# Kernel tuning notes

Measured on AMD Instinct MI355X. Metric: run time of the kernel, lower is better.

Reference implementation:

```python
import jax, jax.numpy as jnp
import numpy as np

D_MODEL = 1024
N_HEADS = 16
D_FF = 2 * D_MODEL
EPS = 1e-6


def setup_inputs() -> dict:
    key = jax.random.key(0)
    ks = jax.random.split(key, 12)
    B, S, D = 2, 2048, D_MODEL
    w = lambda k, shape: (jax.random.normal(k, shape, dtype=jnp.float32) * 0.02)
    return {
        "x": jax.random.normal(ks[0], (B, S, D), dtype=jnp.float32),
        "mask": jnp.ones((B, S, S), dtype=jnp.int32),
        "alpha1": jnp.ones((D,), jnp.float32),
        "bias1": jnp.zeros((D,), jnp.float32),
        "Wq": w(ks[1], (D, D)), "bq": jnp.zeros((D,), jnp.float32),
        "Wk": w(ks[2], (D, D)), "bk": jnp.zeros((D,), jnp.float32),
        "Wv": w(ks[3], (D, D)), "bv": jnp.zeros((D,), jnp.float32),
        "Wo": w(ks[4], (D, D)), "bo": jnp.zeros((D,), jnp.float32),
        "alpha2": jnp.ones((D,), jnp.float32),
        "bias2": jnp.zeros((D,), jnp.float32),
        "W1": w(ks[5], (D, D_FF)), "b1": jnp.zeros((D_FF,), jnp.float32),
        "W2": w(ks[6], (D_FF, D)), "b2": jnp.zeros((D,), jnp.float32),
    }


def _norm(x, alpha, bias):
    # torch: alpha*(x-mean)/(std+eps)+bias, std is unbiased (ddof=1)
    mu = jnp.mean(x, axis=-1, keepdims=True)
    sd = jnp.std(x, axis=-1, ddof=1, keepdims=True)
    return alpha * (x - mu) / (sd + EPS) + bias


def _gelu(x):
    return jax.nn.gelu(x, approximate=False)  # torch F.gelu exact


def _attention(x2, mask, Wq, bq, Wk, bk, Wv, bv, Wo, bo):
    B, S, D = x2.shape
    h, dk = N_HEADS, D // N_HEADS
    # project and split heads: [B, h, S, dk]
    q = (x2 @ Wq + bq).reshape(B, S, h, dk).transpose(0, 2, 1, 3)
    k = (x2 @ Wk + bk).reshape(B, S, h, dk).transpose(0, 2, 1, 3)
    v = (x2 @ Wv + bv).reshape(B, S, h, dk).transpose(0, 2, 1, 3)
    scores = jnp.einsum('bhqd,bhkd->bhqk', q, k) / np.sqrt(dk).astype(np.float32)
    scores = jnp.where(mask[:, None] == 0, jnp.float32(-1e9), scores)
    attn = jax.nn.softmax(scores, axis=-1)
    out = jnp.einsum('bhqk,bhkd->bhqd', attn, v)
    out = out.transpose(0, 2, 1, 3).reshape(B, S, D)
    return out @ Wo + bo


def reference(x, mask, alpha1, bias1, Wq, bq, Wk, bk, Wv, bv, Wo, bo,
              alpha2, bias2, W1, b1, W2, b2):
    x2 = _norm(x, alpha1, bias1)
    x = x + _attention(x2, mask, Wq, bq, Wk, bk, Wv, bv, Wo, bo)
    x2 = _norm(x, alpha2, bias2)
    ff = _gelu(_gelu(x2 @ W1 + b1) @ W2 + b2)
    return x + ff
```

## Files before the change

kernel.cpp:

```cpp
#include <hip/hip_runtime.h>
#include <math.h>

typedef __attribute__((ext_vector_type(8))) short v8s;
typedef __attribute__((ext_vector_type(4))) float v4f;
typedef __attribute__((ext_vector_type(2))) float v2f;
typedef __attribute__((ext_vector_type(16))) float v16f;
typedef __attribute__((ext_vector_type(4))) unsigned int v4u;
typedef __attribute__((ext_vector_type(2))) unsigned int v2u;

#define MFMA16(a,b,c) __builtin_amdgcn_mfma_f32_16x16x32_bf16(a,b,c,0,0,0)
#define MFMA32(a,b,c) __builtin_amdgcn_mfma_f32_32x32x16_bf16(a,b,c,0,0,0)
#define QSCALE 0.18033688011112042f

typedef const __attribute__((address_space(1))) void* gp1_t;
typedef __attribute__((address_space(3))) void* lp3_t;
__device__ __forceinline__ void gll16(const void* g, void* l){
  __builtin_amdgcn_global_load_lds((gp1_t)g, (lp3_t)l, 16, 0, 0);
}
#define VMCNT(n) asm volatile("s_waitcnt vmcnt(" #n ")" ::: "memory")

__device__ __forceinline__ unsigned short f2b(float f){
  unsigned u = __builtin_bit_cast(unsigned, f);
  u += 0x7FFFu + ((u>>16)&1u);
  return (unsigned short)(u>>16);
}
__device__ __forceinline__ float b2f(unsigned short u){
  return __builtin_bit_cast(float, ((unsigned)u)<<16);
}
__device__ __forceinline__ unsigned cvtpk(float lo, float hi){
  unsigned r;
  asm("v_cvt_pk_bf16_f32 %0, %1, %2" : "=v"(r) : "v"(lo), "v"(hi));
  return r;
}
__device__ __forceinline__ float gelu_exact(float x){
  return 0.5f*x*(1.0f + erff(x*0.70710678118654752f));
}

__global__ __launch_bounds__(256) void ln_kernel(const float* __restrict__ x,
    const float* __restrict__ alpha, const float* __restrict__ bias,
    unsigned short* __restrict__ out)
{
  const int D = 1024;
  int row = blockIdx.x;
  int tid = threadIdx.x;
  const float* xr = x + (size_t)row*D;
  v4f v = ((const v4f*)xr)[tid];
  float s  = v[0]+v[1]+v[2]+v[3];
  float s2 = v[0]*v[0]+v[1]*v[1]+v[2]*v[2]+v[3]*v[3];
  #pragma unroll
  for (int off=1; off<64; off<<=1){ s += __shfl_xor(s, off); s2 += __shfl_xor(s2, off); }
  __shared__ float red[8];
  int w = tid>>6;
  if ((tid&63)==0){ red[w]=s; red[4+w]=s2; }
  __syncthreads();
  s  = red[0]+red[1]+red[2]+red[3];
  s2 = red[4]+red[5]+red[6]+red[7];
  float mu  = s*(1.0f/D);
  float var = (s2 - (float)D*mu*mu)*(1.0f/(D-1));
  float inv = 1.0f/(sqrtf(fmaxf(var,0.0f)) + 1e-6f);
  v4f a  = ((const v4f*)alpha)[tid];
  v4f bi = ((const v4f*)bias)[tid];
  unsigned short o[4];
  #pragma unroll
  for (int i=0;i<4;i++) o[i] = f2b(a[i]*(v[i]-mu)*inv + bi[i]);
  v2u pk; pk[0] = (unsigned)o[0] | ((unsigned)o[1]<<16);
          pk[1] = (unsigned)o[2] | ((unsigned)o[3]<<16);
  ((v2u*)(out + (size_t)row*D))[tid] = pk;
}

__global__ __launch_bounds__(256) void transpose_all(
    const float* __restrict__ Wq, const float* __restrict__ Wk,
    const float* __restrict__ Wv, const float* __restrict__ Wo,
    const float* __restrict__ W1, const float* __restrict__ W2,
    unsigned short* __restrict__ wqkvT, unsigned short* __restrict__ woT,
    unsigned short* __restrict__ w1T, unsigned short* __restrict__ w2T)
{
  __shared__ float t[32][33];
  int bid = blockIdx.x;
  const float* in; unsigned short* out; int K, N, idx;
  if (bid < 3072){
    int m = bid >> 10; idx = bid & 1023;
    in = (m==0)?Wq:(m==1)?Wk:Wv; out = wqkvT + (size_t)m*1024*1024; K=1024; N=1024;
  } else if (bid < 4096){ idx = bid-3072; in=Wo; out=woT; K=1024; N=1024; }
  else if (bid < 6144){   idx = bid-4096; in=W1; out=w1T; K=1024; N=2048; }
  else {                  idx = bid-6144; in=W2; out=w2T; K=2048; N=1024; }
  int ntiles = N >> 5;
  int n0 = (idx % ntiles)*32, k0 = (idx / ntiles)*32;
  int tx = threadIdx.x & 31, ty = threadIdx.x >> 5;
  #pragma unroll
  for (int j=0;j<4;j++) t[ty+8*j][tx] = in[(size_t)(k0+ty+8*j)*N + n0+tx];
  __syncthreads();
  #pragma unroll
  for (int j=0;j<4;j++) out[(size_t)(n0+ty+8*j)*K + k0+tx] = f2b(t[tx][ty+8*j]);
}

__global__ __launch_bounds__(256) void mask_flags(const int* __restrict__ mask,
    unsigned char* __restrict__ flags)
{
  const int S = 2048;
  int bid = blockIdx.x;
  int kt = bid & 31, qt = (bid>>5)&31, b = bid>>10;
  int tid = threadIdx.x;
  const int* mp = mask + (size_t)b*S*S + (size_t)(qt*64)*S + kt*64;
  int ok = 1;
  #pragma unroll
  for (int i=0;i<16;i++){
    int idx = tid + i*256;
    int row = idx>>6, col = idx&63;
    ok &= (mp[(size_t)row*S + col] != 0);
  }
  ok = __all(ok) ? 1 : 0;
  __shared__ int f[4];
  if ((tid&63)==0) f[tid>>6] = ok;
  __syncthreads();
  if (tid==0) flags[bid] = (unsigned char)(f[0]&f[1]&f[2]&f[3]);
}

__global__ __launch_bounds__(256) void v_transpose(const unsigned short* __restrict__ vB,
    unsigned short* __restrict__ vT)
{
  __shared__ unsigned short ts[64][68];
  int tt = blockIdx.x & 31, bh = blockIdx.x >> 5;
  int b = bh >> 4, h = bh & 15;
  int tid = threadIdx.x;
  int row = tid>>3, c8 = (tid&7)*8;
  const unsigned short* src = vB + ((size_t)(b*2048 + tt*64))*1024 + h*64;
  #pragma unroll
  for (int j=0;j<2;j++)
    *(v4u*)&ts[row+32*j][c8] = *(const v4u*)(src + (size_t)(row+32*j)*1024 + c8);
  __syncthreads();
  unsigned short* dst = vT + ((size_t)bh*64)*2048 + (size_t)tt*64;
  #pragma unroll
  for (int j=0;j<2;j++){
    int d = row + 32*j;
    unsigned short tmp[8];
    #pragma unroll
    for (int jj=0;jj<8;jj++) tmp[jj] = ts[c8+jj][d];
    *(v4u*)&dst[(size_t)d*2048 + c8] = *(const v4u*)tmp;
  }
}

__global__ __launch_bounds__(256) void gemm_qkv(
    const unsigned short* __restrict__ A, const unsigned short* __restrict__ Bt,
    const float* __restrict__ bq, const float* __restrict__ bk, const float* __restrict__ bv,
    unsigned short* __restrict__ qB, unsigned short* __restrict__ kB, unsigned short* __restrict__ vB)
{
  const int K = 1024, N = 1024;
  __shared__ unsigned short As[3][128][32];
  __shared__ unsigned short Bs[3][128][32];
  int m0 = blockIdx.x*128;
  int ny = blockIdx.y;
  int seg = ny>>3;
  int n0g = ny*128;
  int tid = threadIdx.x;
  int w = tid>>6, l = tid&63;
  int wm = (w>>1)*64, wn = (w&1)*64;
  int r16 = l&15, kq = l>>4;
  v4f acc[4][4] = {};
  int t4 = tid>>2, c8 = (tid&3)*8;
  const unsigned short* Ag = A  + (size_t)(m0 + t4)*K + c8;
  const unsigned short* Bg = Bt + (size_t)(n0g + t4)*K + c8;
  auto stageG = [&](int kb, int idx){
    char* a = (char*)&As[idx][0][0] + w*1024;
    char* b = (char*)&Bs[idx][0][0] + w*1024;
    gll16(Ag + kb,                a);
    gll16(Ag + (size_t)64*K + kb, a + 4096);
    gll16(Bg + kb,                b);
    gll16(Bg + (size_t)64*K + kb, b + 4096);
  };
  const int nk = K/32;
  stageG(0, 0); stageG(32, 1);
  for (int i=0; i<nk; i++){
    int cur = i%3;
    if (i+1 < nk) VMCNT(4); else VMCNT(0);
    __builtin_amdgcn_s_barrier();
    if (i+2 < nk) stageG((i+2)*32, (i+2)%3);
    v8s a[4], b[4];
    #pragma unroll
    for (int mi=0;mi<4;mi++) a[mi] = *(const v8s*)&As[cur][wm+mi*16+r16][kq*8];
    #pragma unroll
    for (int ni=0;ni<4;ni++) b[ni] = *(const v8s*)&Bs[cur][wn+ni*16+r16][kq*8];
    #pragma unroll
    for (int mi=0;mi<4;mi++)
      #pragma unroll
      for (int ni=0;ni<4;ni++)
        acc[mi][ni] = MFMA16(a[mi], b[ni], acc[mi][ni]);
  }
  unsigned short* ob = (seg==0) ? qB : (seg==1) ? kB : vB;
  const float*    bp = (seg==0) ? bq : (seg==1) ? bk : bv;
  float sc = (seg==0) ? QSCALE : 1.0f;
  int ncol0 = (ny&7)*128;
  #pragma unroll
  for (int mi=0;mi<4;mi++){
    #pragma unroll
    for (int ni=0;ni<4;ni++){
      int col = ncol0 + wn + ni*16 + r16;
      float bvv = bp[col];
      #pragma unroll
      for (int r=0;r<4;r++){
        int row = m0 + wm + mi*16 + kq*4 + r;
        ob[(size_t)row*N + col] = f2b((acc[mi][ni][r] + bvv)*sc);
      }
    }
  }
}

template<int MODE>
__global__ __launch_bounds__(256) void gemm64_bt(
    const unsigned short* __restrict__ A, const unsigned short* __restrict__ Bt,
    const float* __restrict__ bias, const float* __restrict__ res,
    unsigned short* __restrict__ outb, float* __restrict__ outf,
    int M, int N, int K)
{
  __shared__ unsigned short As[3][64][32];
  __shared__ unsigned short Bs[3][128][32];
  int m0 = blockIdx.x*64, n0 = blockIdx.y*128;
  int tid = threadIdx.x;
  int w = tid>>6, l = tid&63;
  int wm = (w>>1)*32, wn = (w&1)*64;
  int r16 = l&15, kq = l>>4;
  v4f acc[2][4] = {};
  int t4 = tid>>2, c8 = (tid&3)*8;
  const unsigned short* Ag = A  + (size_t)(m0 + t4)*K + c8;
  const unsigned short* Bg = Bt + (size_t)(n0 + t4)*K + c8;
  auto stageG = [&](int kb, int idx){
    char* a = (char*)&As[idx][0][0] + w*1024;
    char* b = (char*)&Bs[idx][0][0] + w*1024;
    gll16(Ag + kb,                a);
    gll16(Bg + kb,                b);
    gll16(Bg + (size_t)64*K + kb, b + 4096);
  };
  const int nk = K/32;
  stageG(0, 0); stageG(32, 1);
  for (int i=0; i<nk; i++){
    int cur = i%3;
    if (i+1 < nk) VMCNT(3); else VMCNT(0);
    __builtin_amdgcn_s_barrier();
    if (i+2 < nk) stageG((i+2)*32, (i+2)%3);
    v8s a[2], b[4];
    #pragma unroll
    for (int mi=0;mi<2;mi++) a[mi] = *(const v8s*)&As[cur][wm+mi*16+r16][kq*8];
    #pragma unroll
    for (int ni=0;ni<4;ni++) b[ni] = *(const v8s*)&Bs[cur][wn+ni*16+r16][kq*8];
    #pragma unroll
    for (int mi=0;mi<2;mi++)
      #pragma unroll
      for (int ni=0;ni<4;ni++)
        acc[mi][ni] = MFMA16(a[mi], b[ni], acc[mi][ni]);
  }
  #pragma unroll
  for (int mi=0;mi<2;mi++){
    #pragma unroll
    for (int ni=0;ni<4;ni++){
      int col = n0 + wn + ni*16 + r16;
      float bv = bias[col];
      #pragma unroll
      for (int r=0;r<4;r++){
        int row = m0 + wm + mi*16 + kq*4 + r;
        float t = acc[mi][ni][r] + bv;
        if (MODE==2 || MODE==3) t = gelu_exact(t);
        if (MODE==2) outb[(size_t)row*N + col] = f2b(t);
        else         outf[(size_t)row*N + col] = t + res[(size_t)row*N + col];
      }
    }
  }
}

__global__ __launch_bounds__(256, 4) void attn_kernel(
    const unsigned short* __restrict__ Q, const unsigned short* __restrict__ Kb,
    const unsigned short* __restrict__ vT, const int* __restrict__ mask,
    const unsigned char* __restrict__ flags,
    unsigned short* __restrict__ Opart, float* __restrict__ ml)
{
  const int S = 2048, D = 1024;
  __shared__ unsigned short Kb2[2][64][64];
  __shared__ unsigned short Vb2[2][64][64];
  int bid = (blockIdx.x & 7)*128 + (blockIdx.x >> 3);
  int half = bid & 1;
  int qt = (bid >> 1) & 15;
  int bh = bid >> 5;
  int b = bh >> 4, h = bh & 15;
  int tid = threadIdx.x, w = tid>>6, l = tid&63;
  int l31 = l & 31, hi = l >> 5;
  int pidx = (l ^ 32) << 2;
  const unsigned short* Qp  = Q  + (size_t)b*S*D + h*64;
  const unsigned short* Kp  = Kb + (size_t)b*S*D + h*64;
  const unsigned short* vTp = vT + (size_t)bh*64*S;
  int qrow = qt*128 + w*32 + l31;
  v8s qfr[4];
  #pragma unroll
  for (int ks=0;ks<4;ks++)
    qfr[ks] = *(const v8s*)(Qp + (size_t)qrow*D + ks*16 + hi*8);
  float m_run = -1e30f, l_run = 0.0f;
  v16f o0 = {}, o1 = {};
  const int* mp = mask + (size_t)b*S*S;
  const unsigned char* fl = flags + ((size_t)b*32 + qt*2)*32;
  int kt0 = half*16;
  unsigned long long okmask = __ballot( l < 16 ? ((fl[kt0+l] & fl[32+kt0+l]) != 0) : 1 );

  int srow = l>>3;
  int gsw  = (l&7) ^ srow;
  auto stage = [&](int ktg, int idx){
    int kt64 = ktg*64;
    #pragma unroll
    for (int sub=0; sub<2; sub++){
      int row = w*16 + sub*8 + srow;
      gll16(Kp  + (size_t)(kt64+row)*D + gsw*8, &Kb2[idx][w*16+sub*8][0]);
      gll16(vTp + (size_t)row*S + kt64 + gsw*8, &Vb2[idx][w*16+sub*8][0]);
    }
  };
  auto bfrag = [&](unsigned a0, unsigned a1, unsigned a4, unsigned a5) -> v8s {
    unsigned p0 = (unsigned)__builtin_amdgcn_ds_bpermute(pidx, (int)a0);
    unsigned p1 = (unsigned)__builtin_amdgcn_ds_bpermute(pidx, (int)a1);
    unsigned p4 = (unsigned)__builtin_amdgcn_ds_bpermute(pidx, (int)a4);
    unsigned p5 = (unsigned)__builtin_amdgcn_ds_bpermute(pidx, (int)a5);
    v4u pw;
    pw[0] = hi ? p4 : a0;
    pw[1] = hi ? p5 : a1;
    pw[2] = hi ? a4 : p0;
    pw[3] = hi ? a5 : p1;
    return __builtin_bit_cast(v8s, pw);
  };

  stage(kt0, 0);
  int cur = 0;
  for (int it=0; it<16; it++){
    __syncthreads();
    if (it+1 < 16) stage(kt0+it+1, cur^1);
    int ktg = kt0 + it;
    int l7 = l & 7;
    v16f s0 = {}, s1 = {};
    __builtin_amdgcn_s_setprio(1);
    #pragma unroll
    for (int ks=0; ks<4; ks++){
      v8s kf0 = *(const v8s*)&Kb2[cur][l31     ][(((ks*2) + hi) ^ l7)*8];
      v8s kf1 = *(const v8s*)&Kb2[cur][32 + l31][(((ks*2) + hi) ^ l7)*8];
      s0 = MFMA32(kf0, qfr[ks], s0);
      s1 = MFMA32(kf1, qfr[ks], s1);
    }
    __builtin_amdgcn_s_setprio(0);
    if (((~okmask) >> it) & 1ull){
      #pragma unroll
      for (int r=0;r<16;r++){
        int kvl = (r&3) + 8*(r>>2) + 4*hi;
        if (mp[(size_t)qrow*S + ktg*64 + kvl]      == 0) s0[r] = -3.0e38f;
        if (mp[(size_t)qrow*S + ktg*64 + 32 + kvl] == 0) s1[r] = -3.0e38f;
      }
    }
    float t0 = fmaxf(fmaxf(fmaxf(s0[0],s0[1]),fmaxf(s0[2],s0[3])),
                     fmaxf(fmaxf(s0[4],s0[5]),fmaxf(s0[6],s0[7])));
    float t1 = fmaxf(fmaxf(fmaxf(s0[8],s0[9]),fmaxf(s0[10],s0[11])),
                     fmaxf(fmaxf(s0[12],s0[13]),fmaxf(s0[14],s0[15])));
    float t2 = fmaxf(fmaxf(fmaxf(s1[0],s1[1]),fmaxf(s1[2],s1[3])),
                     fmaxf(fmaxf(s1[4],s1[5]),fmaxf(s1[6],s1[7])));
    float t3 = fmaxf(fmaxf(fmaxf(s1[8],s1[9]),fmaxf(s1[10],s1[11])),
                     fmaxf(fmaxf(s1[12],s1[13]),fmaxf(s1[14],s1[15])));
    float tm = fmaxf(fmaxf(t0,t1), fmaxf(t2,t3));
    tm = fmaxf(tm, __shfl_xor(tm, 32));
    if (!__all(tm <= m_run + 11.5f)){
      float mn = fmaxf(m_run, tm);
      float corr = exp2f(m_run - mn);
      m_run = mn;
      l_run *= corr;
      #pragma unroll
      for (int r=0;r<16;r++){ o0[r] *= corr; o1[r] *= corr; }
    }
    #pragma unroll
    for (int r=0;r<16;r++){
      s0[r] = exp2f(s0[r] - m_run);
      s1[r] = exp2f(s1[r] - m_run);
    }
    float a0 = ((s0[0]+s0[1])+(s0[2]+s0[3])) + ((s0[4]+s0[5])+(s0[6]+s0[7]));
    float a1 = ((s0[8]+s0[9])+(s0[10]+s0[11])) + ((s0[12]+s0[13])+(s0[14]+s0[15]));
    float a2 = ((s1[0]+s1[1])+(s1[2]+s1[3])) + ((s1[4]+s1[5])+(s1[6]+s1[7]));
    float a3 = ((s1[8]+s1[9])+(s1[10]+s1[11])) + ((s1[12]+s1[13])+(s1[14]+s1[15]));
    float rs = (a0+a1) + (a2+a3);
    rs += __shfl_xor(rs, 32);
    l_run += rs;
    v8s pb0 = bfrag(cvtpk(s0[0],s0[1]),  cvtpk(s0[2],s0[3]),
                    cvtpk(s0[4],s0[5]),  cvtpk(s0[6],s0[7]));
    v8s pb1 = bfrag(cvtpk(s0[8],s0[9]),  cvtpk(s0[10],s0[11]),
                    cvtpk(s0[12],s0[13]),cvtpk(s0[14],s0[15]));
    v8s pb2 = bfrag(cvtpk(s1[0],s1[1]),  cvtpk(s1[2],s1[3]),
                    cvtpk(s1[4],s1[5]),  cvtpk(s1[6],s1[7]));
    v8s pb3 = bfrag(cvtpk(s1[8],s1[9]),  cvtpk(s1[10],s1[11]),
                    cvtpk(s1[12],s1[13]),cvtpk(s1[14],s1[15]));
    __builtin_amdgcn_s_setprio(1);
    #pragma unroll
    for (int kvs=0; kvs<4; kvs++){
      v8s pb = (kvs==0) ? pb0 : (kvs==1) ? pb1 : (kvs==2) ? pb2 : pb3;
      v8s vv0 = *(const v8s*)&Vb2[cur][l31     ][(((kvs*2) + hi) ^ l7)*8];
      v8s vv1 = *(const v8s*)&Vb2[cur][32 + l31][(((kvs*2) + hi) ^ l7)*8];
      o0 = MFMA32(vv0, pb, o0);
      o1 = MFMA32(vv1, pb, o1);
    }
    __builtin_amdgcn_s_setprio(0);
    cur ^= 1;
  }
  int rowg = b*S + qrow;
  unsigned short* Op = Opart + (size_t)half*4096*1024 + (size_t)rowg*1024 + h*64;
  #pragma unroll
  for (int p=0; p<8; p++){
    int dk = (p&1)*2 + 8*(p>>1) + 4*hi;
    *(unsigned*)(Op + dk)      = cvtpk(o0[2*p], o0[2*p+1]);
    *(unsigned*)(Op + 32 + dk) = cvtpk(o1[2*p], o1[2*p+1]);
  }
  if (!hi){
    float* mlp = ml + ((size_t)half*4096 + rowg)*32 + h*2;
    mlp[0] = m_run;
    mlp[1] = l_run;
  }
}

__global__ __launch_bounds__(256) void attn_combine(const unsigned short* __restrict__ Opart,
    const float* __restrict__ ml, unsigned short* __restrict__ outB)
{
  int row = blockIdx.x;
  int t = threadIdx.x;
  int col = t*4;
  int head = col >> 6;
  const float* m1p = ml + (size_t)row*32 + head*2;
  const float* m2p = ml + ((size_t)4096 + row)*32 + head*2;
  float m1 = m1p[0], l1 = m1p[1];
  float m2 = m2p[0], l2 = m2p[1];
  float M = fmaxf(m1, m2);
  float w1 = exp2f(m1 - M), w2 = exp2f(m2 - M);
  float inv = 1.0f / (l1*w1 + l2*w2);
  v2u au = *(const v2u*)(Opart + (size_t)row*1024 + col);
  v2u bu = *(const v2u*)(Opart + (size_t)4096*1024 + (size_t)row*1024 + col);
  float a0 = b2f((unsigned short)(au[0]&0xffff)), a1 = b2f((unsigned short)(au[0]>>16));
  float a2 = b2f((unsigned short)(au[1]&0xffff)), a3 = b2f((unsigned short)(au[1]>>16));
  float c0 = b2f((unsigned short)(bu[0]&0xffff)), c1 = b2f((unsigned short)(bu[0]>>16));
  float c2 = b2f((unsigned short)(bu[1]&0xffff)), c3 = b2f((unsigned short)(bu[1]>>16));
  v2u pk;
  pk[0] = cvtpk((a0*w1 + c0*w2)*inv, (a1*w1 + c1*w2)*inv);
  pk[1] = cvtpk((a2*w1 + c2*w2)*inv, (a3*w1 + c3*w2)*inv);
  *(v2u*)(outB + (size_t)row*1024 + col) = pk;
}

extern "C" void kernel_launch(void* const* d_in, const int* in_sizes, int n_in,
                              void* d_out, int out_size, void* d_ws, size_t ws_size,
                              hipStream_t stream)
{
  const int D=1024, DFF=2048, BS=4096;
  const float* x      = (const float*)d_in[0];
  const int*   mask   = (const int*)d_in[1];
  const float* alpha1 = (const float*)d_in[2];
  const float* bias1  = (const float*)d_in[3];
  const float* Wq     = (const float*)d_in[4];
  const float* bq     = (const float*)d_in[5];
  const float* Wk     = (const float*)d_in[6];
  const float* bk     = (const float*)d_in[7];
  const float* Wv     = (const float*)d_in[8];
  const float* bv     = (const float*)d_in[9];
  const float* Wo     = (const float*)d_in[10];
  const float* bo     = (const float*)d_in[11];
  const float* alpha2 = (const float*)d_in[12];
  const float* bias2  = (const float*)d_in[13];
  const float* W1     = (const float*)d_in[14];
  const float* b1     = (const float*)d_in[15];
  const float* W2     = (const float*)d_in[16];
  const float* b2     = (const float*)d_in[17];
  float* outp = (float*)d_out;

  char* ws = (char*)d_ws;
  size_t off = 0;
  auto alloc = [&](size_t bytes){ void* p = ws+off; off += (bytes+255)&~(size_t)255; return p; };
  unsigned short* x2b    = (unsigned short*)alloc((size_t)BS*D*2);
  unsigned short* qB     = (unsigned short*)alloc((size_t)BS*D*2);
  unsigned short* kB     = (unsigned short*)alloc((size_t)BS*D*2);
  unsigned short* vB     = (unsigned short*)alloc((size_t)BS*D*2);
  unsigned short* attnB  = (unsigned short*)alloc((size_t)BS*D*2);
  unsigned short* h1     = (unsigned short*)alloc((size_t)BS*DFF*2);
  float*          xres   = (float*)alloc((size_t)BS*D*4);
  unsigned short* wqkvT  = (unsigned short*)alloc((size_t)3*D*D*2);
  unsigned short* woT    = (unsigned short*)alloc((size_t)D*D*2);
  unsigned short* w1T    = (unsigned short*)alloc((size_t)D*DFF*2);
  unsigned short* w2T    = (unsigned short*)alloc((size_t)DFF*D*2);
  unsigned char*  flg    = (unsigned char*)alloc(2048);
  unsigned short* Opart  = (unsigned short*)alloc((size_t)2*BS*D*2);
  float*          mlbuf  = (float*)alloc((size_t)2*BS*16*2*4);
  unsigned short* vTb    = x2b;

  transpose_all<<<8192, 256, 0, stream>>>(Wq, Wk, Wv, Wo, W1, W2,
                                          wqkvT, woT, w1T, w2T);
  mask_flags<<<2048, 256, 0, stream>>>(mask, flg);
  ln_kernel<<<BS, 256, 0, stream>>>(x, alpha1, bias1, x2b);

  gemm_qkv<<<dim3(BS/128, 24), 256, 0, stream>>>(x2b, wqkvT, bq, bk, bv, qB, kB, vB);

  v_transpose<<<1024, 256, 0, stream>>>(vB, vTb);

  attn_kernel<<<1024, 256, 0, stream>>>(qB, kB, vTb, mask, flg, Opart, mlbuf);
  attn_combine<<<4096, 256, 0, stream>>>(Opart, mlbuf, attnB);

  gemm64_bt<1><<<dim3(BS/64, D/128), 256, 0, stream>>>(attnB, woT, bo, x, nullptr, xres, BS, D, D);

  ln_kernel<<<BS, 256, 0, stream>>>(xres, alpha2, bias2, x2b);

  gemm64_bt<2><<<dim3(BS/64, DFF/128), 256, 0, stream>>>(x2b, w1T, b1, nullptr, h1, nullptr, BS, DFF, D);
  gemm64_bt<3><<<dim3(BS/64, D/128), 256, 0, stream>>>(h1, w2T, b2, xres, nullptr, outp, BS, D, DFF);
}
```

Before: 246.4 us.

## Merge preprocessing kernels and write V transposed from QKV GEMM epilogue

Combines weight transpose, mask-flag computation and the first layernorm into one launch by partitioning the block index range. The QKV GEMM epilogue now writes V directly in per-head transposed layout, which removes the separate v_transpose kernel and its extra read and write of V. This cuts two kernel launches and one intermediate pass over V. The transposed V stores are 8-byte writes strided by 2048 elements, so they may be less coalesced than the original row-major stores.

```diff
diff --git a/kernel.cpp b/kernel.cpp
--- a/kernel.cpp
+++ b/kernel.cpp
@@ -68,82 +68,86 @@
   ((v2u*)(out + (size_t)row*D))[tid] = pk;
 }
 
-__global__ __launch_bounds__(256) void transpose_all(
+__global__ __launch_bounds__(256) void preprocess(
     const float* __restrict__ Wq, const float* __restrict__ Wk,
     const float* __restrict__ Wv, const float* __restrict__ Wo,
     const float* __restrict__ W1, const float* __restrict__ W2,
+    const int* __restrict__ mask, const float* __restrict__ x,
+    const float* __restrict__ alpha1, const float* __restrict__ bias1,
     unsigned short* __restrict__ wqkvT, unsigned short* __restrict__ woT,
-    unsigned short* __restrict__ w1T, unsigned short* __restrict__ w2T)
+    unsigned short* __restrict__ w1T, unsigned short* __restrict__ w2T,
+    unsigned char* __restrict__ flags, unsigned short* __restrict__ x2b)
 {
   __shared__ float t[32][33];
+  __shared__ float red[8];
+  __shared__ int f[4];
   int bid = blockIdx.x;
-  const float* in; unsigned short* out; int K, N, idx;
-  if (bid < 3072){
-    int m = bid >> 10; idx = bid & 1023;
-    in = (m==0)?Wq:(m==1)?Wk:Wv; out = wqkvT + (size_t)m*1024*1024; K=1024; N=1024;
-  } else if (bid < 4096){ idx = bid-3072; in=Wo; out=woT; K=1024; N=1024; }
-  else if (bid < 6144){   idx = bid-4096; in=W1; out=w1T; K=1024; N=2048; }
-  else {                  idx = bid-6144; in=W2; out=w2T; K=2048; N=1024; }
-  int ntiles = N >> 5;
-  int n0 = (idx % ntiles)*32, k0 = (idx / ntiles)*32;
-  int tx = threadIdx.x & 31, ty = threadIdx.x >> 5;
-  #pragma unroll
-  for (int j=0;j<4;j++) t[ty+8*j][tx] = in[(size_t)(k0+ty+8*j)*N + n0+tx];
-  __syncthreads();
-  #pragma unroll
-  for (int j=0;j<4;j++) out[(size_t)(n0+ty+8*j)*K + k0+tx] = f2b(t[tx][ty+8*j]);
-}
-
-__global__ __launch_bounds__(256) void mask_flags(const int* __restrict__ mask,
-    unsigned char* __restrict__ flags)
-{
-  const int S = 2048;
-  int bid = blockIdx.x;
-  int kt = bid & 31, qt = (bid>>5)&31, b = bid>>10;
   int tid = threadIdx.x;
-  const int* mp = mask + (size_t)b*S*S + (size_t)(qt*64)*S + kt*64;
-  int ok = 1;
-  #pragma unroll
-  for (int i=0;i<16;i++){
-    int idx = tid + i*256;
-    int row = idx>>6, col = idx&63;
-    ok &= (mp[(size_t)row*S + col] != 0);
-  }
-  ok = __all(ok) ? 1 : 0;
-  __shared__ int f[4];
-  if ((tid&63)==0) f[tid>>6] = ok;
-  __syncthreads();
-  if (tid==0) flags[bid] = (unsigned char)(f[0]&f[1]&f[2]&f[3]);
-}
-
-__global__ __launch_bounds__(256) void v_transpose(const unsigned short* __restrict__ vB,
-    unsigned short* __restrict__ vT)
-{
-  __shared__ unsigned short ts[64][68];
-  int tt = blockIdx.x & 31, bh = blockIdx.x >> 5;
-  int b = bh >> 4, h = bh & 15;
-  int tid = threadIdx.x;
-  int row = tid>>3, c8 = (tid&7)*8;
-  const unsigned short* src = vB + ((size_t)(b*2048 + tt*64))*1024 + h*64;
-  #pragma unroll
-  for (int j=0;j<2;j++)
-    *(v4u*)&ts[row+32*j][c8] = *(const v4u*)(src + (size_t)(row+32*j)*1024 + c8);
-  __syncthreads();
-  unsigned short* dst = vT + ((size_t)bh*64)*2048 + (size_t)tt*64;
-  #pragma unroll
-  for (int j=0;j<2;j++){
-    int d = row + 32*j;
-    unsigned short tmp[8];
-    #pragma unroll
-    for (int jj=0;jj<8;jj++) tmp[jj] = ts[c8+jj][d];
-    *(v4u*)&dst[(size_t)d*2048 + c8] = *(const v4u*)tmp;
+  if (bid < 8192){
+    const float* in; unsigned short* out; int K, N, idx;
+    if (bid < 3072){
+      int m = bid >> 10; idx = bid & 1023;
+      in = (m==0)?Wq:(m==1)?Wk:Wv; out = wqkvT + (size_t)m*1024*1024; K=1024; N=1024;
+    } else if (bid < 4096){ idx = bid-3072; in=Wo; out=woT; K=1024; N=1024; }
+    else if (bid < 6144){   idx = bid-4096; in=W1; out=w1T; K=1024; N=2048; }
+    else {                  idx = bid-6144; in=W2; out=w2T; K=2048; N=1024; }
+    int ntiles = N >> 5;
+    int n0 = (idx % ntiles)*32, k0 = (idx / ntiles)*32;
+    int tx = tid & 31, ty = tid >> 5;
+    #pragma unroll
+    for (int j=0;j<4;j++) t[ty+8*j][tx] = in[(size_t)(k0+ty+8*j)*N + n0+tx];
+    __syncthreads();
+    #pragma unroll
+    for (int j=0;j<4;j++) out[(size_t)(n0+ty+8*j)*K + k0+tx] = f2b(t[tx][ty+8*j]);
+  } else if (bid < 10240){
+    const int S = 2048;
+    int idx = bid - 8192;
+    int kt = idx & 31, qt = (idx>>5)&31, b = idx>>10;
+    const int* mp = mask + (size_t)b*S*S + (size_t)(qt*64)*S + kt*64;
+    int ok = 1;
+    #pragma unroll
+    for (int i=0;i<16;i++){
+      int e = tid + i*256;
+      int row = e>>6, col = e&63;
+      ok &= (mp[(size_t)row*S + col] != 0);
+    }
+    ok = __all(ok) ? 1 : 0;
+    if ((tid&63)==0) f[tid>>6] = ok;
+    __syncthreads();
+    if (tid==0) flags[idx] = (unsigned char)(f[0]&f[1]&f[2]&f[3]);
+  } else {
+    const int D = 1024;
+    int row = bid - 10240;
+    const float* xr = x + (size_t)row*D;
+    v4f v = ((const v4f*)xr)[tid];
+    float s  = v[0]+v[1]+v[2]+v[3];
+    float s2 = v[0]*v[0]+v[1]*v[1]+v[2]*v[2]+v[3]*v[3];
+    #pragma unroll
+    for (int off=1; off<64; off<<=1){ s += __shfl_xor(s, off); s2 += __shfl_xor(s2, off); }
+    int w = tid>>6;
+    if ((tid&63)==0){ red[w]=s; red[4+w]=s2; }
+    __syncthreads();
+    s  = red[0]+red[1]+red[2]+red[3];
+    s2 = red[4]+red[5]+red[6]+red[7];
+    float mu  = s*(1.0f/D);
+    float var = (s2 - (float)D*mu*mu)*(1.0f/(D-1));
+    float inv = 1.0f/(sqrtf(fmaxf(var,0.0f)) + 1e-6f);
+    v4f a  = ((const v4f*)alpha1)[tid];
+    v4f bi = ((const v4f*)bias1)[tid];
+    unsigned short o[4];
+    #pragma unroll
+    for (int i=0;i<4;i++) o[i] = f2b(a[i]*(v[i]-mu)*inv + bi[i]);
+    v2u pk; pk[0] = (unsigned)o[0] | ((unsigned)o[1]<<16);
+            pk[1] = (unsigned)o[2] | ((unsigned)o[3]<<16);
+    ((v2u*)(x2b + (size_t)row*D))[tid] = pk;
   }
 }
 
 __global__ __launch_bounds__(256) void gemm_qkv(
     const unsigned short* __restrict__ A, const unsigned short* __restrict__ Bt,
     const float* __restrict__ bq, const float* __restrict__ bk, const float* __restrict__ bv,
-    unsigned short* __restrict__ qB, unsigned short* __restrict__ kB, unsigned short* __restrict__ vB)
+    unsigned short* __restrict__ qB, unsigned short* __restrict__ kB,
+    unsigned short* __restrict__ vT)
 {
   const int K = 1024, N = 1024;
   __shared__ unsigned short As[3][128][32];
@@ -186,20 +190,38 @@
       for (int ni=0;ni<4;ni++)
         acc[mi][ni] = MFMA16(a[mi], b[ni], acc[mi][ni]);
   }
-  unsigned short* ob = (seg==0) ? qB : (seg==1) ? kB : vB;
-  const float*    bp = (seg==0) ? bq : (seg==1) ? bk : bv;
-  float sc = (seg==0) ? QSCALE : 1.0f;
   int ncol0 = (ny&7)*128;
-  #pragma unroll
-  for (int mi=0;mi<4;mi++){
-    #pragma unroll
-    for (int ni=0;ni<4;ni++){
-      int col = ncol0 + wn + ni*16 + r16;
-      float bvv = bp[col];
-      #pragma unroll
-      for (int r=0;r<4;r++){
-        int row = m0 + wm + mi*16 + kq*4 + r;
-        ob[(size_t)row*N + col] = f2b((acc[mi][ni][r] + bvv)*sc);
+  if (seg < 2){
+    unsigned short* ob = (seg==0) ? qB : kB;
+    const float*    bp = (seg==0) ? bq : bk;
+    float sc = (seg==0) ? QSCALE : 1.0f;
+    #pragma unroll
+    for (int mi=0;mi<4;mi++){
+      #pragma unroll
+      for (int ni=0;ni<4;ni++){
+        int col = ncol0 + wn + ni*16 + r16;
+        float bvv = bp[col];
+        #pragma unroll
+        for (int r=0;r<4;r++){
+          int row = m0 + wm + mi*16 + kq*4 + r;
+          ob[(size_t)row*N + col] = f2b((acc[mi][ni][r] + bvv)*sc);
+        }
+      }
+    }
+  } else {
+    #pragma unroll
+    for (int mi=0;mi<4;mi++){
+      #pragma unroll
+      for (int ni=0;ni<4;ni++){
+        int col = ncol0 + wn + ni*16 + r16;
+        int hh = col >> 6, dk = col & 63;
+        float bvv = bv[col];
+        int row = m0 + wm + mi*16 + kq*4;
+        int bb = row >> 11, s = row & 2047;
+        v2u pk;
+        pk[0] = cvtpk(acc[mi][ni][0]+bvv, acc[mi][ni][1]+bvv);
+        pk[1] = cvtpk(acc[mi][ni][2]+bvv, acc[mi][ni][3]+bvv);
+        *(v2u*)(vT + ((size_t)(bb*16+hh)*64 + dk)*2048 + s) = pk;
       }
     }
   }
@@ -469,7 +491,7 @@
   unsigned short* x2b    = (unsigned short*)alloc((size_t)BS*D*2);
   unsigned short* qB     = (unsigned short*)alloc((size_t)BS*D*2);
   unsigned short* kB     = (unsigned short*)alloc((size_t)BS*D*2);
-  unsigned short* vB     = (unsigned short*)alloc((size_t)BS*D*2);
+  unsigned short* vT     = (unsigned short*)alloc((size_t)BS*D*2);
   unsigned short* attnB  = (unsigned short*)alloc((size_t)BS*D*2);
   unsigned short* h1     = (unsigned short*)alloc((size_t)BS*DFF*2);
   float*          xres   = (float*)alloc((size_t)BS*D*4);
@@ -480,18 +502,14 @@
   unsigned char*  flg    = (unsigned char*)alloc(2048);
   unsigned short* Opart  = (unsigned short*)alloc((size_t)2*BS*D*2);
   float*          mlbuf  = (float*)alloc((size_t)2*BS*16*2*4);
-  unsigned short* vTb    = x2b;
-
-  transpose_all<<<8192, 256, 0, stream>>>(Wq, Wk, Wv, Wo, W1, W2,
-                                          wqkvT, woT, w1T, w2T);
-  mask_flags<<<2048, 256, 0, stream>>>(mask, flg);
-  ln_kernel<<<BS, 256, 0, stream>>>(x, alpha1, bias1, x2b);
-
-  gemm_qkv<<<dim3(BS/128, 24), 256, 0, stream>>>(x2b, wqkvT, bq, bk, bv, qB, kB, vB);
-
-  v_transpose<<<1024, 256, 0, stream>>>(vB, vTb);
-
-  attn_kernel<<<1024, 256, 0, stream>>>(qB, kB, vTb, mask, flg, Opart, mlbuf);
+
+  preprocess<<<14336, 256, 0, stream>>>(Wq, Wk, Wv, Wo, W1, W2,
+                                        mask, x, alpha1, bias1,
+                                        wqkvT, woT, w1T, w2T, flg, x2b);
+
+  gemm_qkv<<<dim3(BS/128, 24), 256, 0, stream>>>(x2b, wqkvT, bq, bk, bv, qB, kB, vT);
+
+  attn_kernel<<<1024, 256, 0, stream>>>(qB, kB, vT, mask, flg, Opart, mlbuf);
   attn_combine<<<4096, 256, 0, stream>>>(Opart, mlbuf, attnB);
 
   gemm64_bt<1><<<dim3(BS/64, D/128), 256, 0, stream>>>(attnB, woT, bo, x, nullptr, xres, BS, D, D);
```

Result: no change. 250.0 us (+1.4%).
